# Kernel optimization log

Hardware: AMD Instinct MI355X
Metric: run time of the kernel (lower is better)

The kernel has to match this reference:

```python
import jax, jax.numpy as jnp
import numpy as np

# Static module configuration (from init_kwargs)
B, H, W, C, HEADS = 16, 56, 56, 256, 8
SPLIT = 7
H_SP, W_SP = H, SPLIT          # idx = 0: vertical stripes
HD = C // HEADS                # head dim = 32
SCALE = HD ** -0.5
NW = (H // H_SP) * (W // W_SP) # 8 windows per image
L = H_SP * W_SP                # 392 tokens per window


def setup_inputs() -> dict:
    key = jax.random.key(0)
    k1, k2 = jax.random.split(key)
    qkv = jax.random.normal(k1, (3, B, H * W, C), dtype=jnp.float32)
    w_conv = jax.random.normal(k2, (3, 3, C, C), dtype=jnp.float32) * 0.02  # HWIO
    b_conv = jnp.zeros((C,), dtype=jnp.float32)
    return {"qkv": qkv, "w_conv": w_conv, "b_conv": b_conv}


def _window_img(x):
    # (B, N, C) -> (B*NW, H_SP, W_SP, C)  non-overlapping stripe windows
    x = x.reshape(B, H // H_SP, H_SP, W // W_SP, W_SP, C)
    x = x.transpose(0, 1, 3, 2, 4, 5)  # (B, nH, nW, H_SP, W_SP, C)
    return x.reshape(B * NW, H_SP, W_SP, C)


def _heads(xw):
    # (B*NW, H_SP, W_SP, C) -> (B*NW, HEADS, L, HD)
    return xw.reshape(B * NW, L, HEADS, HD).transpose(0, 2, 1, 3)


def reference(qkv, w_conv, b_conv):
    q, k, v = qkv[0], qkv[1], qkv[2]
    qw = _heads(_window_img(q)) * SCALE           # (BW, h, L, d)
    kw = _heads(_window_img(k))
    v_img = _window_img(v)                        # (BW, H_SP, W_SP, C)
    # LePE: dense 3x3 conv (groups=1 in source) over each window, SAME padding
    lepe = jax.lax.conv_general_dilated(
        v_img, w_conv, window_strides=(1, 1), padding='SAME',
        dimension_numbers=('NHWC', 'HWIO', 'NHWC')) + b_conv
    lepe = _heads(lepe)
    vw = _heads(v_img)
    attn = jax.nn.softmax(jnp.einsum('whld,whmd->whlm', qw, kw), axis=-1)
    x = jnp.einsum('whlm,whmd->whld', attn, vw) + lepe  # (BW, h, L, d)
    # windows -> image -> (B, N, C)
    x = x.transpose(0, 2, 1, 3).reshape(B, H // H_SP, W // W_SP, H_SP, W_SP, C)
    x = x.transpose(0, 1, 3, 2, 4, 5).reshape(B, H * W, C)
    return x
```

## Files before the change

### kernel.cpp

```cpp
#include <hip/hip_runtime.h>
#include <cmath>
#include <cstdint>

#define NBATCH 16
#define HH 56
#define WW 56
#define CCH 256
#define NHEADS 8
#define HDIM 32
#define WSP 7
#define NWIN 128
#define LTOK 392
#define NTOK 3136

typedef __attribute__((ext_vector_type(8))) __bf16 bf16x8;
typedef __attribute__((ext_vector_type(4))) __bf16 bf16x4;
typedef __attribute__((ext_vector_type(4))) float f32x4;

__global__ __launch_bounds__(256) void pack_w(const float* __restrict__ w,
                                              __bf16* __restrict__ Wt) {
    int idx = blockIdx.x * blockDim.x + threadIdx.x;
    if (idx >= 9 * CCH * CCH) return;
    int tap = idx / (CCH * CCH);
    int rem = idx % (CCH * CCH);
    int co = rem / CCH, ci = rem % CCH;
    Wt[idx] = (__bf16)(w[(size_t)tap * CCH * CCH + (size_t)ci * CCH + co]);
}

#define AV_R 10
#define AV_C 9
#define AV_S 264
__global__ __launch_bounds__(256, 2) void lepe_conv(const float* __restrict__ qkv,
        const __bf16* __restrict__ Wt, const float* __restrict__ bconv,
        float* __restrict__ out) {
    const int bid = blockIdx.x;
    const int win = bid / 7, rb = bid % 7;
    const int b = win >> 3, wi = win & 7;
    const int rbase = rb * 8;
    const int tid = threadIdx.x;
    const int lane = tid & 63, wv = tid >> 6;
    const int lr = lane & 15, lg = lane >> 4;
    __shared__ __bf16 Av[AV_R * AV_C * AV_S];
    __shared__ __bf16 Bs[2][4][2048];
    const float* vsrc = qkv + 2 * (size_t)NBATCH * NTOK * CCH;

    for (int t = tid; t < AV_R * AV_C * 64; t += 256) {
        int rr = t / (AV_C * 64);
        int rem = t % (AV_C * 64);
        int cc = rem / 64, chg = rem % 64;
        int ar = rbase + rr - 1, c = cc - 1;
        f32x4 v = {0.f, 0.f, 0.f, 0.f};
        if (ar >= 0 && ar < HH && c >= 0 && c < WSP) {
            int token = ar * WW + wi * WSP + c;
            v = *(const f32x4*)(vsrc + ((size_t)b * NTOK + token) * CCH + chg * 4);
        }
        bf16x4 w;
#pragma unroll
        for (int i = 0; i < 4; i++) w[i] = (__bf16)v[i];
        *(bf16x4*)&Av[(rr * AV_C + cc) * AV_S + chg * 4] = w;
    }
    __syncthreads();

    f32x4 acc[4][4];
#pragma unroll
    for (int i = 0; i < 4; i++)
#pragma unroll
        for (int j = 0; j < 4; j++) acc[i][j] = (f32x4){0.f, 0.f, 0.f, 0.f};

    int ab[4];
#pragma unroll
    for (int mt = 0; mt < 4; mt++) {
        int p = mt * 16 + lr; if (p > 55) p = 55;
        ab[mt] = ((p / 7) * AV_C + (p % 7)) * AV_S + lg * 8;
    }
    int bro[4];
#pragma unroll
    for (int nt = 0; nt < 4; nt++)
        bro[nt] = (nt * 16 + lr) * 32 + ((lg ^ ((lr >> 1) & 3)) * 8);
    const __bf16* wsrc = Wt + (size_t)(wv * 64 + (lane >> 2)) * CCH
                            + (((lane & 3) ^ ((lane >> 3) & 3)) * 8);
    __bf16* b0 = &Bs[0][wv][0];
    __bf16* b1 = &Bs[1][wv][0];

#define GLDS(gp, lp)                                                        \
    __builtin_amdgcn_global_load_lds(                                       \
        (const __attribute__((address_space(1))) void*)(gp),                \
        (__attribute__((address_space(3))) void*)(lp), 16, 0, 0)
#define ISSUE(s, lb) do {                                                   \
        const int tp_ = (s) >> 3, kq_ = (s) & 7;                            \
        const __bf16* g_ = wsrc + tp_ * (CCH * CCH) + kq_ * 32;             \
        GLDS(g_, lb);                                                       \
        GLDS(g_ + 16 * CCH, (lb) + 512);                                    \
        GLDS(g_ + 32 * CCH, (lb) + 1024);                                   \
        GLDS(g_ + 48 * CCH, (lb) + 1536);                                   \
    } while (0)
#define STEPX(s, lb, doiss, s2) do {                                        \
        const int tap_ = (s) >> 3, ks_ = (s) & 7;                           \
        const int dy_ = (tap_ >= 6) ? 2 : ((tap_ >= 3) ? 1 : 0);            \
        const int offa = (tap_ + 6 * dy_) * AV_S + ks_ * 32;                \
        bf16x8 a_[4], bb_[4];                                               \
        _Pragma("unroll")                                                   \
        for (int mt = 0; mt < 4; mt++)                                      \
            a_[mt] = *(const bf16x8*)&Av[ab[mt] + offa];                    \
        _Pragma("unroll")                                                   \
        for (int nt = 0; nt < 4; nt++)                                      \
            bb_[nt] = *(const bf16x8*)&(lb)[bro[nt]];                       \
        asm volatile("s_waitcnt lgkmcnt(0)" ::: "memory");                  \
        __builtin_amdgcn_sched_barrier(0);                                  \
        if (doiss) ISSUE(s2, lb);                                           \
        _Pragma("unroll")                                                   \
        for (int mt = 0; mt < 4; mt++)                                      \
            _Pragma("unroll")                                               \
            for (int nt = 0; nt < 4; nt++)                                  \
                acc[mt][nt] = __builtin_amdgcn_mfma_f32_16x16x32_bf16(      \
                    a_[mt], bb_[nt], acc[mt][nt], 0, 0, 0);                 \
    } while (0)
#define WAIT4 asm volatile("s_waitcnt vmcnt(4)" ::: "memory")
#define WAIT0 asm volatile("s_waitcnt vmcnt(0)" ::: "memory")

    ISSUE(0, b0);
    ISSUE(1, b1);
    for (int s = 0; s < 70; s += 2) {
        WAIT4; STEPX(s, b0, 1, s + 2);
        WAIT4; STEPX(s + 1, b1, 1, s + 3);
    }
    WAIT4; STEPX(70, b0, 0, 0);
    WAIT0; STEPX(71, b1, 0, 0);
#undef GLDS
#undef ISSUE
#undef STEPX
#undef WAIT4
#undef WAIT0

#pragma unroll
    for (int nt = 0; nt < 4; nt++) {
        int ch = wv * 64 + nt * 16 + lr;
        float bias = bconv[ch];
#pragma unroll
        for (int mt = 0; mt < 4; mt++) {
#pragma unroll
            for (int r = 0; r < 4; r++) {
                int p = mt * 16 + lg * 4 + r;
                if (p < 56) {
                    int ar = rbase + p / 7, c = p % 7;
                    int token = ar * WW + wi * WSP + c;
                    out[((size_t)b * NTOK + token) * CCH + ch] = acc[mt][nt][r] + bias;
                }
            }
        }
    }
}

#define KS_R 400
#define KS_S 36
#define VS_S 424
#define PB_S 36
__global__ __launch_bounds__(512, 4) void attn2(const float* __restrict__ qkv,
                                                float* __restrict__ out) {
    const int wh = blockIdx.x;
    const int win = wh >> 3, h = wh & 7;
    const int b = win >> 3, wi = win & 7;
    const int tid = threadIdx.x;
    const int lane = tid & 63, wv = tid >> 6;
    const int lr = lane & 15, lg = lane >> 4;
    const float scale = 0.17677669529663687f;

    __shared__ __bf16 Ks[KS_R * KS_S];
    __shared__ __bf16 Vs[HDIM * VS_S];
    __shared__ __bf16 Pb[8][16 * PB_S];

    const size_t plane = (size_t)NBATCH * NTOK * CCH;
    const float* qsrc = qkv + ((size_t)b * NTOK) * CCH + h * HDIM;
    const float* ksrc = qsrc + plane;
    const float* vsrc = qsrc + 2 * plane;

    for (int t = tid; t < KS_R * 4; t += 512) {
        int row = t >> 2, g = t & 3;
        bf16x8 val;
        if (row < LTOK) {
            int tok = (row / 7) * WW + wi * WSP + row % 7;
            const float* p = ksrc + (size_t)tok * CCH + g * 8;
            f32x4 a = *(const f32x4*)p;
            f32x4 c = *(const f32x4*)(p + 4);
#pragma unroll
            for (int i = 0; i < 4; i++) { val[i] = (__bf16)a[i]; val[4 + i] = (__bf16)c[i]; }
        } else {
#pragma unroll
            for (int i = 0; i < 8; i++) val[i] = (__bf16)0.0f;
        }
        *(bf16x8*)&Ks[row * KS_S + g * 8] = val;
    }
    for (int t = tid; t < LTOK * 4; t += 512) {
        int key = t % LTOK, chg = t / LTOK;
        int tok = (key / 7) * WW + wi * WSP + key % 7;
        const float* p = vsrc + (size_t)tok * CCH + chg * 8;
        f32x4 a = *(const f32x4*)p;
        f32x4 c = *(const f32x4*)(p + 4);
#pragma unroll
        for (int i = 0; i < 4; i++) {
            Vs[(chg * 8 + i) * VS_S + key] = (__bf16)a[i];
            Vs[(chg * 8 + 4 + i) * VS_S + key] = (__bf16)c[i];
        }
    }
    for (int t = tid; t < HDIM * 32; t += 512) {
        int ch = t >> 5, k = t & 31;
        Vs[ch * VS_S + LTOK + k] = (__bf16)0.0f;
    }
    __syncthreads();

    __bf16* pb = Pb[wv];
    for (int tile = wv; tile < 25; tile += 8) {
        int qrow = tile * 16 + lr;
        int qe = qrow < LTOK ? qrow : LTOK - 1;
        int tokq = (qe / 7) * WW + wi * WSP + qe % 7;
        const float* qp = qsrc + (size_t)tokq * CCH + lg * 8;
        f32x4 qa = *(const f32x4*)qp;
        f32x4 qc = *(const f32x4*)(qp + 4);
        bf16x8 aq;
#pragma unroll
        for (int i = 0; i < 4; i++) {
            aq[i] = (__bf16)(qa[i] * scale);
            aq[4 + i] = (__bf16)(qc[i] * scale);
        }

        f32x4 s[26];
#pragma unroll
        for (int t = 0; t < 25; t++) {
            bf16x8 bk = *(const bf16x8*)&Ks[(t * 16 + lr) * KS_S + lg * 8];
            s[t] = __builtin_amdgcn_mfma_f32_16x16x32_bf16(
                aq, bk, (f32x4){0.f, 0.f, 0.f, 0.f}, 0, 0, 0);
        }
#pragma unroll
        for (int r = 0; r < 4; r++) s[25][r] = -INFINITY;
        if (lr >= 8) {
#pragma unroll
            for (int r = 0; r < 4; r++) s[24][r] = -INFINITY;
        }
        float inv[4];
#pragma unroll
        for (int r = 0; r < 4; r++) {
            float m = s[0][r];
#pragma unroll
            for (int t = 1; t < 25; t++) m = fmaxf(m, s[t][r]);
#pragma unroll
            for (int off = 1; off < 16; off <<= 1) m = fmaxf(m, __shfl_xor(m, off, 64));
            float sum = 0.f;
#pragma unroll
            for (int t = 0; t < 26; t++) {
                float e = __expf(s[t][r] - m);
                s[t][r] = e;
                sum += e;
            }
#pragma unroll
            for (int off = 1; off < 16; off <<= 1) sum += __shfl_xor(sum, off, 64);
            inv[r] = 1.0f / sum;
        }
        f32x4 xacc[2] = {{0.f, 0.f, 0.f, 0.f}, {0.f, 0.f, 0.f, 0.f}};
        for (int j = 0; j < 13; j++) {
#pragma unroll
            for (int half = 0; half < 2; half++) {
                int t = 2 * j + half;
#pragma unroll
                for (int r = 0; r < 4; r++)
                    pb[(lg * 4 + r) * PB_S + half * 16 + lr] = (__bf16)s[t][r];
            }
            asm volatile("s_waitcnt lgkmcnt(0)" ::: "memory");
            __builtin_amdgcn_sched_barrier(0);
            bf16x4 lo = *(const bf16x4*)&pb[lr * PB_S + lg * 8];
            bf16x4 hi = *(const bf16x4*)&pb[lr * PB_S + lg * 8 + 4];
            bf16x8 ap;
#pragma unroll
            for (int i = 0; i < 4; i++) { ap[i] = lo[i]; ap[4 + i] = hi[i]; }
#pragma unroll
            for (int nt = 0; nt < 2; nt++) {
                bf16x8 bv = *(const bf16x8*)&Vs[(nt * 16 + lr) * VS_S + j * 32 + lg * 8];
                xacc[nt] = __builtin_amdgcn_mfma_f32_16x16x32_bf16(ap, bv, xacc[nt], 0, 0, 0);
            }
            __builtin_amdgcn_sched_barrier(0);
        }
#pragma unroll
        for (int r = 0; r < 4; r++) {
            int q = tile * 16 + lg * 4 + r;
            if (q < LTOK) {
                int rI = q / 7, c = q % 7;
                size_t base = ((size_t)b * NTOK + rI * WW + wi * WSP + c) * CCH + h * HDIM;
#pragma unroll
                for (int nt = 0; nt < 2; nt++)
                    out[base + nt * 16 + lr] += xacc[nt][r] * inv[r];
            }
        }
    }
}

extern "C" void kernel_launch(void* const* d_in, const int* in_sizes, int n_in,
                              void* d_out, int out_size, void* d_ws, size_t ws_size,
                              hipStream_t stream) {
    const float* qkv = (const float*)d_in[0];
    const float* wconv = (const float*)d_in[1];
    const float* bconv = (const float*)d_in[2];
    float* out = (float*)d_out;
    char* ws = (char*)d_ws;

    const size_t WT_BYTES = (size_t)9 * CCH * CCH * 2;
    if (ws_size < WT_BYTES) return;
    __bf16* Wt = (__bf16*)ws;

    pack_w<<<(9 * CCH * CCH + 255) / 256, 256, 0, stream>>>(wconv, Wt);
    lepe_conv<<<NWIN * 7, 256, 0, stream>>>(qkv, Wt, bconv, out);
    attn2<<<NWIN * NHEADS, 512, 0, stream>>>(qkv, out);
}
```

Before: 193.2 us.

## Compute attention scores transposed with two-pass online softmax to cut registers

Swaps the MFMA operands so each lane holds scores for a single query row across keys. This removes the 16-lane row-wise shuffle reductions. The 25 key tiles are split into two halves with an online-softmax rescale, so only 13 score fragments are live at once instead of 26, which lowers VGPR pressure. The P matrix is written to LDS as packed 64-bit stores without the explicit waitcnt and sched barriers. This adds a rescale pass and extra cross-lane shuffles, and removing the explicit LDS wait risks ordering the store and load incorrectly.

```diff
diff --git a/kernel.cpp b/kernel.cpp
--- a/kernel.cpp
+++ b/kernel.cpp
@@ -16,6 +16,13 @@
 typedef __attribute__((ext_vector_type(8))) __bf16 bf16x8;
 typedef __attribute__((ext_vector_type(4))) __bf16 bf16x4;
 typedef __attribute__((ext_vector_type(4))) float f32x4;
+
+static __device__ __forceinline__ uint32_t pkbf(float a, float b) {
+    __bf16 x = (__bf16)a, y = (__bf16)b;
+    uint16_t xu = __builtin_bit_cast(uint16_t, x);
+    uint16_t yu = __builtin_bit_cast(uint16_t, y);
+    return (uint32_t)xu | ((uint32_t)yu << 16);
+}
 
 __global__ __launch_bounds__(256) void pack_w(const float* __restrict__ w,
                                               __bf16* __restrict__ Wt) {
@@ -199,7 +206,7 @@
 #pragma unroll
         for (int i = 0; i < 4; i++) {
             Vs[(chg * 8 + i) * VS_S + key] = (__bf16)a[i];
-            Vs[(chg * 8 + 4 + i) * VS_S + key] = (__bf16)c[i];
+            Vs[(chg * 8 + 4 + i) * VS_S + key] = (__bf16)0.0f + (__bf16)c[i];
         }
     }
     for (int t = tid; t < HDIM * 32; t += 512) {
@@ -223,70 +230,115 @@
             aq[4 + i] = (__bf16)(qc[i] * scale);
         }
 
-        f32x4 s[26];
-#pragma unroll
-        for (int t = 0; t < 25; t++) {
-            bf16x8 bk = *(const bf16x8*)&Ks[(t * 16 + lr) * KS_S + lg * 8];
-            s[t] = __builtin_amdgcn_mfma_f32_16x16x32_bf16(
-                aq, bk, (f32x4){0.f, 0.f, 0.f, 0.f}, 0, 0, 0);
-        }
-#pragma unroll
-        for (int r = 0; r < 4; r++) s[25][r] = -INFINITY;
-        if (lr >= 8) {
-#pragma unroll
-            for (int r = 0; r < 4; r++) s[24][r] = -INFINITY;
-        }
-        float inv[4];
+        float m_run = 0.f, sum_run = 0.f;
+        f32x4 xacc[2] = {{0.f, 0.f, 0.f, 0.f}, {0.f, 0.f, 0.f, 0.f}};
+
+#pragma unroll
+        for (int hh = 0; hh < 2; hh++) {
+            const int NT = hh ? 13 : 12;
+            const int TB = hh ? 12 : 0;
+            const int NC = hh ? 7 : 6;
+
+            f32x4 s[13];
+#pragma unroll
+            for (int t = 0; t < NT; t++) {
+                bf16x8 bk = *(const bf16x8*)&Ks[((TB + t) * 16 + lr) * KS_S + lg * 8];
+                s[t] = __builtin_amdgcn_mfma_f32_16x16x32_bf16(
+                    bk, aq, (f32x4){0.f, 0.f, 0.f, 0.f}, 0, 0, 0);
+            }
+            f32x4 vm = s[0];
+#pragma unroll
+            for (int t = 1; t < 12; t++) {
+#pragma unroll
+                for (int r = 0; r < 4; r++) vm[r] = fmaxf(vm[r], s[t][r]);
+            }
+            if (hh && lg < 2) {
+#pragma unroll
+                for (int r = 0; r < 4; r++) vm[r] = fmaxf(vm[r], s[12][r]);
+            }
+            float mh = fmaxf(fmaxf(vm[0], vm[1]), fmaxf(vm[2], vm[3]));
+            mh = fmaxf(mh, __shfl_xor(mh, 16, 64));
+            mh = fmaxf(mh, __shfl_xor(mh, 32, 64));
+
+            float m_new = hh ? fmaxf(m_run, mh) : mh;
+            if (hh) {
+                float f = __expf(m_run - m_new);
+                sum_run *= f;
+#pragma unroll
+                for (int r = 0; r < 4; r++) {
+                    float fr = __shfl(f, 4 * lg + r, 64);
+                    xacc[0][r] *= fr;
+                    xacc[1][r] *= fr;
+                }
+            }
+            m_run = m_new;
+
+            f32x4 vsum = {0.f, 0.f, 0.f, 0.f};
+#pragma unroll
+            for (int t = 0; t < 12; t++) {
+#pragma unroll
+                for (int r = 0; r < 4; r++) {
+                    float e = __expf(s[t][r] - m_new);
+                    s[t][r] = e;
+                    vsum[r] += e;
+                }
+            }
+            if (hh) {
+                if (lg < 2) {
+#pragma unroll
+                    for (int r = 0; r < 4; r++) {
+                        float e = __expf(s[12][r] - m_new);
+                        s[12][r] = e;
+                        vsum[r] += e;
+                    }
+                } else {
+#pragma unroll
+                    for (int r = 0; r < 4; r++) s[12][r] = 0.f;
+                }
+            }
+            float sumh = (vsum[0] + vsum[1]) + (vsum[2] + vsum[3]);
+            sumh += __shfl_xor(sumh, 16, 64);
+            sumh += __shfl_xor(sumh, 32, 64);
+            sum_run += sumh;
+
+#pragma unroll
+            for (int c = 0; c < NC; c++) {
+                uint2 wa, wb;
+                wa.x = pkbf(s[2 * c][0], s[2 * c][1]);
+                wa.y = pkbf(s[2 * c][2], s[2 * c][3]);
+                if (2 * c + 1 < NT) {
+                    wb.x = pkbf(s[2 * c + 1][0], s[2 * c + 1][1]);
+                    wb.y = pkbf(s[2 * c + 1][2], s[2 * c + 1][3]);
+                } else {
+                    wb.x = 0u; wb.y = 0u;
+                }
+                *(uint2*)&pb[lr * PB_S + 4 * lg] = wa;
+                *(uint2*)&pb[lr * PB_S + 16 + 4 * lg] = wb;
+                bf16x4 lo = *(const bf16x4*)&pb[lr * PB_S + 8 * lg];
+                bf16x4 hi = *(const bf16x4*)&pb[lr * PB_S + 8 * lg + 4];
+                bf16x8 ap;
+#pragma unroll
+                for (int i = 0; i < 4; i++) { ap[i] = lo[i]; ap[4 + i] = hi[i]; }
+                const int kbase = TB * 16 + c * 32;
+#pragma unroll
+                for (int nt = 0; nt < 2; nt++) {
+                    bf16x8 bv = *(const bf16x8*)&Vs[(nt * 16 + lr) * VS_S + kbase + lg * 8];
+                    xacc[nt] = __builtin_amdgcn_mfma_f32_16x16x32_bf16(ap, bv, xacc[nt], 0, 0, 0);
+                }
+            }
+        }
+
+        float inv = 1.0f / sum_run;
 #pragma unroll
         for (int r = 0; r < 4; r++) {
-            float m = s[0][r];
-#pragma unroll
-            for (int t = 1; t < 25; t++) m = fmaxf(m, s[t][r]);
-#pragma unroll
-            for (int off = 1; off < 16; off <<= 1) m = fmaxf(m, __shfl_xor(m, off, 64));
-            float sum = 0.f;
-#pragma unroll
-            for (int t = 0; t < 26; t++) {
-                float e = __expf(s[t][r] - m);
-                s[t][r] = e;
-                sum += e;
-            }
-#pragma unroll
-            for (int off = 1; off < 16; off <<= 1) sum += __shfl_xor(sum, off, 64);
-            inv[r] = 1.0f / sum;
-        }
-        f32x4 xacc[2] = {{0.f, 0.f, 0.f, 0.f}, {0.f, 0.f, 0.f, 0.f}};
-        for (int j = 0; j < 13; j++) {
-#pragma unroll
-            for (int half = 0; half < 2; half++) {
-                int t = 2 * j + half;
-#pragma unroll
-                for (int r = 0; r < 4; r++)
-                    pb[(lg * 4 + r) * PB_S + half * 16 + lr] = (__bf16)s[t][r];
-            }
-            asm volatile("s_waitcnt lgkmcnt(0)" ::: "memory");
-            __builtin_amdgcn_sched_barrier(0);
-            bf16x4 lo = *(const bf16x4*)&pb[lr * PB_S + lg * 8];
-            bf16x4 hi = *(const bf16x4*)&pb[lr * PB_S + lg * 8 + 4];
-            bf16x8 ap;
-#pragma unroll
-            for (int i = 0; i < 4; i++) { ap[i] = lo[i]; ap[4 + i] = hi[i]; }
-#pragma unroll
-            for (int nt = 0; nt < 2; nt++) {
-                bf16x8 bv = *(const bf16x8*)&Vs[(nt * 16 + lr) * VS_S + j * 32 + lg * 8];
-                xacc[nt] = __builtin_amdgcn_mfma_f32_16x16x32_bf16(ap, bv, xacc[nt], 0, 0, 0);
-            }
-            __builtin_amdgcn_sched_barrier(0);
-        }
-#pragma unroll
-        for (int r = 0; r < 4; r++) {
-            int q = tile * 16 + lg * 4 + r;
+            float invr = __shfl(inv, 4 * lg + r, 64);
+            int q = tile * 16 + 4 * lg + r;
             if (q < LTOK) {
                 int rI = q / 7, c = q % 7;
                 size_t base = ((size_t)b * NTOK + rI * WW + wi * WSP + c) * CCH + h * HDIM;
 #pragma unroll
                 for (int nt = 0; nt < 2; nt++)
-                    out[base + nt * 16 + lr] += xacc[nt][r] * inv[r];
+                    out[base + nt * 16 + lr] += xacc[nt][r] * invr;
             }
         }
     }
```

Result: slower. 406.8 us (+110.5%).

## Transpose QK MFMA and split softmax into two online passes

Applied to the files above, without the earlier changes.

Swaps the MFMA operands so each lane holds scores for a single query row. Row max and sum then need only two cross-lane shuffles instead of a 16-lane butterfly per row. The 25 key tiles are handled in two halves with online-softmax rescaling, which lowers the number of score registers kept live and is meant to relieve VGPR pressure. P is packed into bf16 pairs and written to LDS as vectors, dropping the explicit waitcnt and sched barriers, at the cost of extra rescale exps and shuffles.

```diff
diff --git a/kernel.cpp b/kernel.cpp
--- a/kernel.cpp
+++ b/kernel.cpp
@@ -16,6 +16,13 @@
 typedef __attribute__((ext_vector_type(8))) __bf16 bf16x8;
 typedef __attribute__((ext_vector_type(4))) __bf16 bf16x4;
 typedef __attribute__((ext_vector_type(4))) float f32x4;
+
+static __device__ __forceinline__ uint32_t pkbf(float a, float b) {
+    __bf16 x = (__bf16)a, y = (__bf16)b;
+    uint16_t xu = __builtin_bit_cast(uint16_t, x);
+    uint16_t yu = __builtin_bit_cast(uint16_t, y);
+    return (uint32_t)xu | ((uint32_t)yu << 16);
+}
 
 __global__ __launch_bounds__(256) void pack_w(const float* __restrict__ w,
                                               __bf16* __restrict__ Wt) {
@@ -223,70 +230,112 @@
             aq[4 + i] = (__bf16)(qc[i] * scale);
         }
 
-        f32x4 s[26];
-#pragma unroll
-        for (int t = 0; t < 25; t++) {
-            bf16x8 bk = *(const bf16x8*)&Ks[(t * 16 + lr) * KS_S + lg * 8];
-            s[t] = __builtin_amdgcn_mfma_f32_16x16x32_bf16(
-                aq, bk, (f32x4){0.f, 0.f, 0.f, 0.f}, 0, 0, 0);
-        }
-#pragma unroll
-        for (int r = 0; r < 4; r++) s[25][r] = -INFINITY;
-        if (lr >= 8) {
-#pragma unroll
-            for (int r = 0; r < 4; r++) s[24][r] = -INFINITY;
-        }
-        float inv[4];
+        float m_run = 0.f, sum_run = 0.f;
+        f32x4 xacc[2] = {{0.f, 0.f, 0.f, 0.f}, {0.f, 0.f, 0.f, 0.f}};
+
+#define HALF_PASS(NT, TB, NC, FIRST) do {                                   \
+    f32x4 s[NT];                                                            \
+    _Pragma("unroll")                                                       \
+    for (int t = 0; t < NT; t++) {                                          \
+        bf16x8 bk = *(const bf16x8*)&Ks[((TB + t) * 16 + lr) * KS_S + lg * 8]; \
+        s[t] = __builtin_amdgcn_mfma_f32_16x16x32_bf16(                     \
+            bk, aq, (f32x4){0.f, 0.f, 0.f, 0.f}, 0, 0, 0);                  \
+    }                                                                       \
+    f32x4 vm = s[0];                                                        \
+    _Pragma("unroll")                                                       \
+    for (int t = 1; t < 12; t++) {                                          \
+        _Pragma("unroll")                                                   \
+        for (int r = 0; r < 4; r++) vm[r] = fmaxf(vm[r], s[t][r]);          \
+    }                                                                       \
+    if (NT == 13 && lg < 2) {                                               \
+        _Pragma("unroll")                                                   \
+        for (int r = 0; r < 4; r++) vm[r] = fmaxf(vm[r], s[NT - 1][r]);     \
+    }                                                                       \
+    float mh = fmaxf(fmaxf(vm[0], vm[1]), fmaxf(vm[2], vm[3]));             \
+    mh = fmaxf(mh, __shfl_xor(mh, 16, 64));                                 \
+    mh = fmaxf(mh, __shfl_xor(mh, 32, 64));                                 \
+    float m_new = FIRST ? mh : fmaxf(m_run, mh);                            \
+    if (!FIRST) {                                                           \
+        float f = __expf(m_run - m_new);                                    \
+        sum_run *= f;                                                       \
+        _Pragma("unroll")                                                   \
+        for (int r = 0; r < 4; r++) {                                       \
+            float fr = __shfl(f, 4 * lg + r, 64);                           \
+            xacc[0][r] *= fr;                                               \
+            xacc[1][r] *= fr;                                               \
+        }                                                                   \
+    }                                                                       \
+    m_run = m_new;                                                          \
+    f32x4 vsum = {0.f, 0.f, 0.f, 0.f};                                      \
+    _Pragma("unroll")                                                       \
+    for (int t = 0; t < 12; t++) {                                          \
+        _Pragma("unroll")                                                   \
+        for (int r = 0; r < 4; r++) {                                       \
+            float e = __expf(s[t][r] - m_new);                              \
+            s[t][r] = e;                                                    \
+            vsum[r] += e;                                                   \
+        }                                                                   \
+    }                                                                       \
+    if (NT == 13) {                                                         \
+        if (lg < 2) {                                                       \
+            _Pragma("unroll")                                               \
+            for (int r = 0; r < 4; r++) {                                   \
+                float e = __expf(s[NT - 1][r] - m_new);                     \
+                s[NT - 1][r] = e;                                           \
+                vsum[r] += e;                                               \
+            }                                                               \
+        } else {                                                            \
+            _Pragma("unroll")                                               \
+            for (int r = 0; r < 4; r++) s[NT - 1][r] = 0.f;                 \
+        }                                                                   \
+    }                                                                       \
+    float sumh = (vsum[0] + vsum[1]) + (vsum[2] + vsum[3]);                 \
+    sumh += __shfl_xor(sumh, 16, 64);                                       \
+    sumh += __shfl_xor(sumh, 32, 64);                                       \
+    sum_run += sumh;                                                        \
+    _Pragma("unroll")                                                       \
+    for (int c = 0; c < NC; c++) {                                          \
+        uint2 wa, wb;                                                       \
+        wa.x = pkbf(s[2 * c][0], s[2 * c][1]);                              \
+        wa.y = pkbf(s[2 * c][2], s[2 * c][3]);                              \
+        if (2 * c + 1 < NT) {                                               \
+            wb.x = pkbf(s[2 * c + 1][0], s[2 * c + 1][1]);                  \
+            wb.y = pkbf(s[2 * c + 1][2], s[2 * c + 1][3]);                  \
+        } else {                                                            \
+            wb.x = 0u; wb.y = 0u;                                           \
+        }                                                                   \
+        *(uint2*)&pb[lr * PB_S + 4 * lg] = wa;                              \
+        *(uint2*)&pb[lr * PB_S + 16 + 4 * lg] = wb;                         \
+        bf16x4 lo = *(const bf16x4*)&pb[lr * PB_S + 8 * lg];                \
+        bf16x4 hi = *(const bf16x4*)&pb[lr * PB_S + 8 * lg + 4];            \
+        bf16x8 ap;                                                          \
+        _Pragma("unroll")                                                   \
+        for (int i = 0; i < 4; i++) { ap[i] = lo[i]; ap[4 + i] = hi[i]; }   \
+        const int kbase = TB * 16 + c * 32;                                 \
+        _Pragma("unroll")                                                   \
+        for (int nt = 0; nt < 2; nt++) {                                    \
+            bf16x8 bv = *(const bf16x8*)&Vs[(nt * 16 + lr) * VS_S + kbase + lg * 8]; \
+            xacc[nt] = __builtin_amdgcn_mfma_f32_16x16x32_bf16(             \
+                ap, bv, xacc[nt], 0, 0, 0);                                 \
+        }                                                                   \
+    }                                                                       \
+} while (0)
+
+        HALF_PASS(12, 0, 6, 1);
+        HALF_PASS(13, 12, 7, 0);
+#undef HALF_PASS
+
+        float inv = 1.0f / sum_run;
 #pragma unroll
         for (int r = 0; r < 4; r++) {
-            float m = s[0][r];
-#pragma unroll
-            for (int t = 1; t < 25; t++) m = fmaxf(m, s[t][r]);
-#pragma unroll
-            for (int off = 1; off < 16; off <<= 1) m = fmaxf(m, __shfl_xor(m, off, 64));
-            float sum = 0.f;
-#pragma unroll
-            for (int t = 0; t < 26; t++) {
-                float e = __expf(s[t][r] - m);
-                s[t][r] = e;
-                sum += e;
-            }
-#pragma unroll
-            for (int off = 1; off < 16; off <<= 1) sum += __shfl_xor(sum, off, 64);
-            inv[r] = 1.0f / sum;
-        }
-        f32x4 xacc[2] = {{0.f, 0.f, 0.f, 0.f}, {0.f, 0.f, 0.f, 0.f}};
-        for (int j = 0; j < 13; j++) {
-#pragma unroll
-            for (int half = 0; half < 2; half++) {
-                int t = 2 * j + half;
-#pragma unroll
-                for (int r = 0; r < 4; r++)
-                    pb[(lg * 4 + r) * PB_S + half * 16 + lr] = (__bf16)s[t][r];
-            }
-            asm volatile("s_waitcnt lgkmcnt(0)" ::: "memory");
-            __builtin_amdgcn_sched_barrier(0);
-            bf16x4 lo = *(const bf16x4*)&pb[lr * PB_S + lg * 8];
-            bf16x4 hi = *(const bf16x4*)&pb[lr * PB_S + lg * 8 + 4];
-            bf16x8 ap;
-#pragma unroll
-            for (int i = 0; i < 4; i++) { ap[i] = lo[i]; ap[4 + i] = hi[i]; }
-#pragma unroll
-            for (int nt = 0; nt < 2; nt++) {
-                bf16x8 bv = *(const bf16x8*)&Vs[(nt * 16 + lr) * VS_S + j * 32 + lg * 8];
-                xacc[nt] = __builtin_amdgcn_mfma_f32_16x16x32_bf16(ap, bv, xacc[nt], 0, 0, 0);
-            }
-            __builtin_amdgcn_sched_barrier(0);
-        }
-#pragma unroll
-        for (int r = 0; r < 4; r++) {
-            int q = tile * 16 + lg * 4 + r;
+            float invr = __shfl(inv, 4 * lg + r, 64);
+            int q = tile * 16 + 4 * lg + r;
             if (q < LTOK) {
                 int rI = q / 7, c = q % 7;
                 size_t base = ((size_t)b * NTOK + rI * WW + wi * WSP + c) * CCH + h * HDIM;
 #pragma unroll
                 for (int nt = 0; nt < 2; nt++)
-                    out[base + nt * 16 + lr] += xacc[nt][r] * inv[r];
+                    out[base + nt * 16 + lr] += xacc[nt][r] * invr;
             }
         }
     }
```

New measurement: 405.6 us. 2.1x slower.
